# Kernel tuning notes

Measured on AMD Instinct MI355X. Metric: run time of the kernel, lower is better.

The kernel has to match this reference:

```python
import jax, jax.numpy as jnp
import numpy as np

NUM_GRAPHS = 1024
N_NODES = 8388608

def setup_inputs() -> dict:
    key = jax.random.key(0)
    k1, k2, k3 = jax.random.split(key, 3)
    positions = jax.random.normal(k1, (N_NODES, 3), dtype=jnp.float32)
    q = jax.random.normal(k2, (N_NODES,), dtype=jnp.float32)
    batch = jnp.sort(jax.random.randint(k3, (N_NODES,), 0, NUM_GRAPHS, dtype=jnp.int64))
    return {"positions": positions, "q": q, "batch": batch}

def reference(positions, q, batch):
    # q: [N] -> [N,1]; remove global mean over all nodes (remove_mean=True)
    qc = q[:, None] - jnp.mean(q)
    # per-graph polarization: sum_i q_i * r_i  -> [NUM_GRAPHS, 3]
    pol = jax.ops.segment_sum(qc * positions, batch, num_segments=NUM_GRAPHS)
    return pol
```

## Files before the change

kernel.cpp:

```cpp
#include <hip/hip_runtime.h>


#define N_NODES         8388608
#define NUM_GRAPHS      1024
#define BLK             256
#define NODES_PER_BLOCK 4096
#define NBLOCKS         (N_NODES / NODES_PER_BLOCK)
#define ITER            4
#define NSLOT           4

#define IBASE_OFF       16
#define SPLIT_OFF       2064
#define REC_OFF         10256
#define REC_STRIDE      32
#define EXTRA_OFF       (REC_OFF + NBLOCKS * REC_STRIDE)
#define WS_FLOATS       (EXTRA_OFF + NUM_GRAPHS * 6)

__global__ __launch_bounds__(BLK) void split_kernel(const int* __restrict__ batch,
                                                    float* __restrict__ ws) {
    int b = blockIdx.x * BLK + threadIdx.x;
    if (b >= NBLOCKS) return;

    float* extra = ws + EXTRA_OFF;
    extra[b * 3 + 0] = 0.f; extra[b * 3 + 1] = 0.f; extra[b * 3 + 2] = 0.f;

    const int s = b * NODES_PER_BLOCK;
    const int e = s + NODES_PER_BLOCK;
    int i0 = batch[s];
    int i1 = batch[e - 1];
    int split = e;
    if (i1 != i0) {
        int lo = s + 1, hi = e - 1;
        while (lo < hi) {
            int mid = (lo + hi) >> 1;
            if (batch[mid] > i0) hi = mid; else lo = mid + 1;
        }
        split = lo;
    }
    ((int4*)(ws + SPLIT_OFF))[b] = make_int4(i0, i1, split, 0);
    ((int*)(ws + IBASE_OFF))[b] = i0;
}

__global__ __launch_bounds__(BLK) void pol_main(const float4* __restrict__ p4,
                                                const float4* __restrict__ q4,
                                                const int*    __restrict__ batch,
                                                float* __restrict__ ws) {
    __shared__ float sslot[NSLOT * 6];
    __shared__ float sqsum;

    const int t = threadIdx.x;
    const int b = blockIdx.x;
    float* extra = ws + EXTRA_OFF;

    const int e = (b + 1) * NODES_PER_BLOCK;
    const int4 si = ((const int4*)(ws + SPLIT_OFF))[b];
    const int i0 = si.x, i1 = si.y, split = si.z;
    const bool general = (i1 > i0 + 1);

    if (t < NSLOT * 6) sslot[t] = 0.f;
    if (t == 0) sqsum = 0.f;
    __syncthreads();

    float4 Q[ITER], P0[ITER], P1[ITER], P2[ITER];
    const int blk_v4 = b * (NODES_PER_BLOCK / 4);
    #pragma unroll
    for (int j = 0; j < ITER; ++j) {
        int vi = blk_v4 + j * BLK + t;
        Q[j]  = q4[vi];
        P0[j] = p4[3 * vi + 0];
        P1[j] = p4[3 * vi + 1];
        P2[j] = p4[3 * vi + 2];
    }

    float aqx = 0, aqy = 0, aqz = 0, arx = 0, ary = 0, arz = 0;
    float bqx = 0, bqy = 0, bqz = 0, brx = 0, bry = 0, brz = 0;
    float qsum = 0.f;

    if (!general) {
        #pragma unroll
        for (int j = 0; j < ITER; ++j) {
            int gidx = (blk_v4 + j * BLK + t) * 4;
            float qs[4] = {Q[j].x, Q[j].y, Q[j].z, Q[j].w};
            float px[4] = {P0[j].x, P0[j].w, P1[j].z, P2[j].y};
            float py[4] = {P0[j].y, P1[j].x, P1[j].w, P2[j].z};
            float pz[4] = {P0[j].z, P1[j].y, P2[j].x, P2[j].w};
            qsum += (qs[0] + qs[1]) + (qs[2] + qs[3]);
            #pragma unroll
            for (int k = 0; k < 4; ++k) {
                if (gidx + k < split) {
                    aqx = fmaf(qs[k], px[k], aqx); aqy = fmaf(qs[k], py[k], aqy);
                    aqz = fmaf(qs[k], pz[k], aqz);
                    arx += px[k]; ary += py[k]; arz += pz[k];
                } else {
                    bqx = fmaf(qs[k], px[k], bqx); bqy = fmaf(qs[k], py[k], bqy);
                    bqz = fmaf(qs[k], pz[k], bqz);
                    brx += px[k]; bry += py[k]; brz += pz[k];
                }
            }
        }
    } else {
        #pragma unroll
        for (int j = 0; j < ITER; ++j) {
            int gidx = (blk_v4 + j * BLK + t) * 4;
            float qs[4] = {Q[j].x, Q[j].y, Q[j].z, Q[j].w};
            float px[4] = {P0[j].x, P0[j].w, P1[j].z, P2[j].y};
            float py[4] = {P0[j].y, P1[j].x, P1[j].w, P2[j].z};
            float pz[4] = {P0[j].z, P1[j].y, P2[j].x, P2[j].w};
            for (int k = 0; k < 4; ++k) {
                int id = batch[gidx + k];
                float qv = qs[k];
                qsum += qv;
                atomicAdd(&extra[id * 6 + 0], qv * px[k]);
                atomicAdd(&extra[id * 6 + 1], qv * py[k]);
                atomicAdd(&extra[id * 6 + 2], qv * pz[k]);
                atomicAdd(&extra[id * 6 + 3], px[k]);
                atomicAdd(&extra[id * 6 + 4], py[k]);
                atomicAdd(&extra[id * 6 + 5], pz[k]);
            }
        }
    }

    #pragma unroll
    for (int off = 32; off > 0; off >>= 1) qsum += __shfl_down(qsum, off, 64);
    if ((t & 63) == 0) atomicAdd(&sqsum, qsum);

    if (!general) {
        #pragma unroll
        for (int off = 32; off > 0; off >>= 1) {
            aqx += __shfl_down(aqx, off, 64); aqy += __shfl_down(aqy, off, 64);
            aqz += __shfl_down(aqz, off, 64); arx += __shfl_down(arx, off, 64);
            ary += __shfl_down(ary, off, 64); arz += __shfl_down(arz, off, 64);
        }
        if ((t & 63) == 0) {
            atomicAdd(&sslot[0], aqx); atomicAdd(&sslot[1], aqy);
            atomicAdd(&sslot[2], aqz); atomicAdd(&sslot[3], arx);
            atomicAdd(&sslot[4], ary); atomicAdd(&sslot[5], arz);
        }
        if (split < e) {
            #pragma unroll
            for (int off = 32; off > 0; off >>= 1) {
                bqx += __shfl_down(bqx, off, 64); bqy += __shfl_down(bqy, off, 64);
                bqz += __shfl_down(bqz, off, 64); brx += __shfl_down(brx, off, 64);
                bry += __shfl_down(bry, off, 64); brz += __shfl_down(brz, off, 64);
            }
            if ((t & 63) == 0) {
                int sl = i1 - i0;
                atomicAdd(&sslot[sl * 6 + 0], bqx); atomicAdd(&sslot[sl * 6 + 1], bqy);
                atomicAdd(&sslot[sl * 6 + 2], bqz); atomicAdd(&sslot[sl * 6 + 3], brx);
                atomicAdd(&sslot[sl * 6 + 4], bry); atomicAdd(&sslot[sl * 6 + 5], brz);
            }
        }
    }
    __syncthreads();

    float* rec = ws + REC_OFF + (size_t)b * REC_STRIDE;
    if (t == 0) rec[0] = sqsum;
    if (t < NSLOT * 6) rec[8 + t] = sslot[t];
}

__global__ __launch_bounds__(1024) void finalize_kernel(const float* __restrict__ ws,
                                                        float* __restrict__ out) {
    __shared__ float sm[16];
    __shared__ float smean;
    const int t = threadIdx.x;

    float s = ws[REC_OFF + (size_t)t * REC_STRIDE]
            + ws[REC_OFF + (size_t)(t + 1024) * REC_STRIDE];
    #pragma unroll
    for (int off = 32; off > 0; off >>= 1) s += __shfl_down(s, off, 64);
    if ((t & 63) == 0) sm[t >> 6] = s;
    __syncthreads();
    if (t == 0) {
        float tot = 0.f;
        #pragma unroll
        for (int i = 0; i < 16; ++i) tot += sm[i];
        smean = tot * (1.0f / (float)N_NODES);
    }
    __syncthreads();
    const float mean = smean;

    const int g = t;
    const int* ibase = (const int*)(ws + IBASE_OFF);
    const float* extra = ws + EXTRA_OFF;

    float qx = extra[g * 6 + 0], qy = extra[g * 6 + 1], qz = extra[g * 6 + 2];
    float rx = extra[g * 6 + 3], ry = extra[g * 6 + 4], rz = extra[g * 6 + 5];

    int lo = 0, hi = NBLOCKS - 1, B = -1;
    while (lo <= hi) {
        int mid = (lo + hi) >> 1;
        if (ibase[mid] <= g) { B = mid; lo = mid + 1; } else hi = mid - 1;
    }
    for (int b = B; b >= 0; --b) {
        int sl = g - ibase[b];
        if (sl >= NSLOT) break;
        const float* p = ws + REC_OFF + (size_t)b * REC_STRIDE + 8 + sl * 6;
        qx += p[0]; qy += p[1]; qz += p[2];
        rx += p[3]; ry += p[4]; rz += p[5];
    }
    out[g * 3 + 0] = fmaf(-mean, rx, qx);
    out[g * 3 + 1] = fmaf(-mean, ry, qy);
    out[g * 3 + 2] = fmaf(-mean, rz, qz);
}


__global__ void sum_q_kernel(const float* __restrict__ q, float* __restrict__ ws, int n4) {
    int tid = blockIdx.x * blockDim.x + threadIdx.x;
    int stride = gridDim.x * blockDim.x;
    const float4* q4 = (const float4*)q;
    float s = 0.f;
    for (int i = tid; i < n4; i += stride) {
        float4 v = q4[i];
        s += (v.x + v.y) + (v.z + v.w);
    }
    for (int off = 32; off > 0; off >>= 1) s += __shfl_down(s, off, 64);
    __shared__ float smem[4];
    int lane = threadIdx.x & 63, wave = threadIdx.x >> 6;
    if (lane == 0) smem[wave] = s;
    __syncthreads();
    if (threadIdx.x == 0) atomicAdd(ws, (smem[0] + smem[1]) + (smem[2] + smem[3]));
}

__global__ void pol_atomic_kernel(const float* __restrict__ pos,
                                  const float* __restrict__ q,
                                  const int*   __restrict__ batch,
                                  const float* __restrict__ ws,
                                  float* __restrict__ out, int n) {
    const float mean = ws[0] * (1.0f / (float)N_NODES);
    int tid = blockIdx.x * blockDim.x + threadIdx.x;
    int stride = gridDim.x * blockDim.x;
    int n4 = n >> 2;
    const float4* q4 = (const float4*)q;
    const int4*   b4 = (const int4*)batch;
    const float4* p4 = (const float4*)pos;

    for (int i = tid; i < n4; i += stride) {
        float4 qv = q4[i];
        int4   bv = b4[i];
        float4 p0 = p4[3 * i + 0];
        float4 p1 = p4[3 * i + 1];
        float4 p2 = p4[3 * i + 2];
        float qs[4] = {qv.x - mean, qv.y - mean, qv.z - mean, qv.w - mean};
        int  ids[4] = {bv.x, bv.y, bv.z, bv.w};
        float px[4] = {p0.x, p0.w, p1.z, p2.y};
        float py[4] = {p0.y, p1.x, p1.w, p2.z};
        float pz[4] = {p0.z, p1.y, p2.x, p2.w};
        int cur = ids[0];
        float sx = 0.f, sy = 0.f, sz = 0.f;
        #pragma unroll
        for (int j = 0; j < 4; ++j) {
            if (ids[j] != cur) {
                atomicAdd(&out[cur * 3 + 0], sx);
                atomicAdd(&out[cur * 3 + 1], sy);
                atomicAdd(&out[cur * 3 + 2], sz);
                sx = sy = sz = 0.f;
                cur = ids[j];
            }
            sx = fmaf(qs[j], px[j], sx);
            sy = fmaf(qs[j], py[j], sy);
            sz = fmaf(qs[j], pz[j], sz);
        }
        int first = __shfl(cur, 0, 64);
        bool uniform = __all(cur == first);
        if (uniform) {
            for (int off = 32; off > 0; off >>= 1) {
                sx += __shfl_down(sx, off, 64);
                sy += __shfl_down(sy, off, 64);
                sz += __shfl_down(sz, off, 64);
            }
            if ((threadIdx.x & 63) == 0) {
                atomicAdd(&out[cur * 3 + 0], sx);
                atomicAdd(&out[cur * 3 + 1], sy);
                atomicAdd(&out[cur * 3 + 2], sz);
            }
        } else {
            atomicAdd(&out[cur * 3 + 0], sx);
            atomicAdd(&out[cur * 3 + 1], sy);
            atomicAdd(&out[cur * 3 + 2], sz);
        }
    }
}

extern "C" void kernel_launch(void* const* d_in, const int* in_sizes, int n_in,
                              void* d_out, int out_size, void* d_ws, size_t ws_size,
                              hipStream_t stream) {
    const float* pos   = (const float*)d_in[0];
    const float* q     = (const float*)d_in[1];
    const int*   batch = (const int*)d_in[2];
    float* out = (float*)d_out;
    float* ws  = (float*)d_ws;
    int n = in_sizes[1];

    if (ws_size >= (size_t)WS_FLOATS * sizeof(float)) {
        split_kernel<<<NBLOCKS / BLK, BLK, 0, stream>>>(batch, ws);
        pol_main<<<NBLOCKS, BLK, 0, stream>>>((const float4*)pos, (const float4*)q,
                                              batch, ws);
        finalize_kernel<<<1, 1024, 0, stream>>>(ws, out);
    } else {
        hipMemsetAsync(d_out, 0, (size_t)out_size * sizeof(float), stream);
        hipMemsetAsync(d_ws, 0, sizeof(float), stream);
        sum_q_kernel<<<4096, BLK, 0, stream>>>(q, ws, n >> 2);
        pol_atomic_kernel<<<8192, BLK, 0, stream>>>(pos, q, batch, ws, out, n);
    }
}
```

Measured before the change: 204.1 us.

## Fuse split search into main kernel and parallelize finalize across blocks

```diff
diff --git a/kernel.cpp b/kernel.cpp
--- a/kernel.cpp
+++ b/kernel.cpp
@@ -9,25 +9,40 @@
 #define ITER            4
 #define NSLOT           4
 
-#define IBASE_OFF       16
-#define SPLIT_OFF       2064
-#define REC_OFF         10256
+#define IBASE_OFF       0
+#define QS_OFF          NBLOCKS
+#define REC_OFF         (2 * NBLOCKS)
 #define REC_STRIDE      32
-#define EXTRA_OFF       (REC_OFF + NBLOCKS * REC_STRIDE)
-#define WS_FLOATS       (EXTRA_OFF + NUM_GRAPHS * 6)
-
-__global__ __launch_bounds__(BLK) void split_kernel(const int* __restrict__ batch,
-                                                    float* __restrict__ ws) {
-    int b = blockIdx.x * BLK + threadIdx.x;
-    if (b >= NBLOCKS) return;
-
-    float* extra = ws + EXTRA_OFF;
-    extra[b * 3 + 0] = 0.f; extra[b * 3 + 1] = 0.f; extra[b * 3 + 2] = 0.f;
+#define WS_FLOATS       (REC_OFF + NBLOCKS * REC_STRIDE)
+
+__global__ __launch_bounds__(BLK) void pol_main(const float4* __restrict__ p4,
+                                                const float4* __restrict__ q4,
+                                                const int*    __restrict__ batch,
+                                                float* __restrict__ ws) {
+    __shared__ float sslot[NSLOT * 6];
+    __shared__ float sqsum;
+
+    const int t = threadIdx.x;
+    const int b = blockIdx.x;
+
+    float4 Q[ITER], P0[ITER], P1[ITER], P2[ITER];
+    const int blk_v4 = b * (NODES_PER_BLOCK / 4);
+    #pragma unroll
+    for (int j = 0; j < ITER; ++j) {
+        int vi = blk_v4 + j * BLK + t;
+        Q[j]  = q4[vi];
+        P0[j] = p4[3 * vi + 0];
+        P1[j] = p4[3 * vi + 1];
+        P2[j] = p4[3 * vi + 2];
+    }
+
+    if (t < NSLOT * 6) sslot[t] = 0.f;
+    if (t == 0) sqsum = 0.f;
 
     const int s = b * NODES_PER_BLOCK;
     const int e = s + NODES_PER_BLOCK;
-    int i0 = batch[s];
-    int i1 = batch[e - 1];
+    const int i0 = batch[s];
+    const int i1 = batch[e - 1];
     int split = e;
     if (i1 != i0) {
         int lo = s + 1, hi = e - 1;
@@ -37,40 +52,9 @@
         }
         split = lo;
     }
-    ((int4*)(ws + SPLIT_OFF))[b] = make_int4(i0, i1, split, 0);
-    ((int*)(ws + IBASE_OFF))[b] = i0;
-}
-
-__global__ __launch_bounds__(BLK) void pol_main(const float4* __restrict__ p4,
-                                                const float4* __restrict__ q4,
-                                                const int*    __restrict__ batch,
-                                                float* __restrict__ ws) {
-    __shared__ float sslot[NSLOT * 6];
-    __shared__ float sqsum;
-
-    const int t = threadIdx.x;
-    const int b = blockIdx.x;
-    float* extra = ws + EXTRA_OFF;
-
-    const int e = (b + 1) * NODES_PER_BLOCK;
-    const int4 si = ((const int4*)(ws + SPLIT_OFF))[b];
-    const int i0 = si.x, i1 = si.y, split = si.z;
     const bool general = (i1 > i0 + 1);
 
-    if (t < NSLOT * 6) sslot[t] = 0.f;
-    if (t == 0) sqsum = 0.f;
-    __syncthreads();
-
-    float4 Q[ITER], P0[ITER], P1[ITER], P2[ITER];
-    const int blk_v4 = b * (NODES_PER_BLOCK / 4);
-    #pragma unroll
-    for (int j = 0; j < ITER; ++j) {
-        int vi = blk_v4 + j * BLK + t;
-        Q[j]  = q4[vi];
-        P0[j] = p4[3 * vi + 0];
-        P1[j] = p4[3 * vi + 1];
-        P2[j] = p4[3 * vi + 2];
-    }
+    __syncthreads();
 
     float aqx = 0, aqy = 0, aqz = 0, arx = 0, ary = 0, arz = 0;
     float bqx = 0, bqy = 0, bqz = 0, brx = 0, bry = 0, brz = 0;
@@ -107,15 +91,17 @@
             float py[4] = {P0[j].y, P1[j].x, P1[j].w, P2[j].z};
             float pz[4] = {P0[j].z, P1[j].y, P2[j].x, P2[j].w};
             for (int k = 0; k < 4; ++k) {
-                int id = batch[gidx + k];
+                int sl = batch[gidx + k] - i0;
                 float qv = qs[k];
                 qsum += qv;
-                atomicAdd(&extra[id * 6 + 0], qv * px[k]);
-                atomicAdd(&extra[id * 6 + 1], qv * py[k]);
-                atomicAdd(&extra[id * 6 + 2], qv * pz[k]);
-                atomicAdd(&extra[id * 6 + 3], px[k]);
-                atomicAdd(&extra[id * 6 + 4], py[k]);
-                atomicAdd(&extra[id * 6 + 5], pz[k]);
+                if (sl < NSLOT) {
+                    atomicAdd(&sslot[sl * 6 + 0], qv * px[k]);
+                    atomicAdd(&sslot[sl * 6 + 1], qv * py[k]);
+                    atomicAdd(&sslot[sl * 6 + 2], qv * pz[k]);
+                    atomicAdd(&sslot[sl * 6 + 3], px[k]);
+                    atomicAdd(&sslot[sl * 6 + 4], py[k]);
+                    atomicAdd(&sslot[sl * 6 + 5], pz[k]);
+                }
             }
         }
     }
@@ -154,47 +140,44 @@
     __syncthreads();
 
     float* rec = ws + REC_OFF + (size_t)b * REC_STRIDE;
-    if (t == 0) rec[0] = sqsum;
-    if (t < NSLOT * 6) rec[8 + t] = sslot[t];
-}
-
-__global__ __launch_bounds__(1024) void finalize_kernel(const float* __restrict__ ws,
+    if (t < NSLOT * 6) rec[t] = sslot[t];
+    if (t == 0) {
+        ws[QS_OFF + b] = sqsum;
+        ((int*)ws)[IBASE_OFF + b] = i0;
+    }
+}
+
+#define FBLK  64
+#define FGRID (NUM_GRAPHS / FBLK)
+
+__global__ __launch_bounds__(FBLK) void finalize_kernel(const float* __restrict__ ws,
                                                         float* __restrict__ out) {
-    __shared__ float sm[16];
-    __shared__ float smean;
+    __shared__ int sbase[NBLOCKS];
     const int t = threadIdx.x;
 
-    float s = ws[REC_OFF + (size_t)t * REC_STRIDE]
-            + ws[REC_OFF + (size_t)(t + 1024) * REC_STRIDE];
-    #pragma unroll
-    for (int off = 32; off > 0; off >>= 1) s += __shfl_down(s, off, 64);
-    if ((t & 63) == 0) sm[t >> 6] = s;
-    __syncthreads();
-    if (t == 0) {
-        float tot = 0.f;
-        #pragma unroll
-        for (int i = 0; i < 16; ++i) tot += sm[i];
-        smean = tot * (1.0f / (float)N_NODES);
-    }
-    __syncthreads();
-    const float mean = smean;
-
-    const int g = t;
-    const int* ibase = (const int*)(ws + IBASE_OFF);
-    const float* extra = ws + EXTRA_OFF;
-
-    float qx = extra[g * 6 + 0], qy = extra[g * 6 + 1], qz = extra[g * 6 + 2];
-    float rx = extra[g * 6 + 3], ry = extra[g * 6 + 4], rz = extra[g * 6 + 5];
-
+    float ssum = 0.f;
+    #pragma unroll
+    for (int j = 0; j < NBLOCKS / FBLK; ++j) ssum += ws[QS_OFF + j * FBLK + t];
+    #pragma unroll
+    for (int off = 32; off > 0; off >>= 1) ssum += __shfl_down(ssum, off, 64);
+    const float mean = __shfl(ssum, 0, 64) * (1.0f / (float)N_NODES);
+
+    const int* ibase = (const int*)ws;
+    #pragma unroll
+    for (int j = 0; j < NBLOCKS / FBLK; ++j) sbase[j * FBLK + t] = ibase[j * FBLK + t];
+    __syncthreads();
+
+    const int g = blockIdx.x * FBLK + t;
     int lo = 0, hi = NBLOCKS - 1, B = -1;
     while (lo <= hi) {
         int mid = (lo + hi) >> 1;
-        if (ibase[mid] <= g) { B = mid; lo = mid + 1; } else hi = mid - 1;
-    }
+        if (sbase[mid] <= g) { B = mid; lo = mid + 1; } else hi = mid - 1;
+    }
+    float qx = 0, qy = 0, qz = 0, rx = 0, ry = 0, rz = 0;
     for (int b = B; b >= 0; --b) {
-        int sl = g - ibase[b];
+        int sl = g - sbase[b];
         if (sl >= NSLOT) break;
-        const float* p = ws + REC_OFF + (size_t)b * REC_STRIDE + 8 + sl * 6;
+        const float* p = ws + REC_OFF + (size_t)b * REC_STRIDE + sl * 6;
         qx += p[0]; qy += p[1]; qz += p[2];
         rx += p[3]; ry += p[4]; rz += p[5];
     }
@@ -292,10 +275,9 @@
     int n = in_sizes[1];
 
     if (ws_size >= (size_t)WS_FLOATS * sizeof(float)) {
-        split_kernel<<<NBLOCKS / BLK, BLK, 0, stream>>>(batch, ws);
         pol_main<<<NBLOCKS, BLK, 0, stream>>>((const float4*)pos, (const float4*)q,
                                               batch, ws);
-        finalize_kernel<<<1, 1024, 0, stream>>>(ws, out);
+        finalize_kernel<<<FGRID, FBLK, 0, stream>>>(ws, out);
     } else {
         hipMemsetAsync(d_out, 0, (size_t)out_size * sizeof(float), stream);
         hipMemsetAsync(d_ws, 0, sizeof(float), stream);
```

After: 192.9 us. 1.06x faster.
